# Kernel tuning notes

Hardware: AMD Instinct MI355X
Metric: run time of the kernel (lower is better)

The kernel has to match this reference:

```python
import jax, jax.numpy as jnp
import numpy as np

D_MODEL = 768
EXPAND = 2
D_INNER = EXPAND * D_MODEL  # 1536
D_STATE = 16
D_CONV = 4
DT_RANK = D_MODEL // 16  # 48
N_LAYER = 3
BATCH, SEQLEN = 2, 1024
EPS = 1e-5


def setup_inputs() -> dict:
    key = jax.random.key(0)
    ks = jax.random.split(key, 8)
    s = 0.02
    hidden_states = jax.random.normal(ks[0], (BATCH, SEQLEN, D_MODEL), jnp.float32)
    norm_w = jnp.ones((N_LAYER, D_MODEL), jnp.float32)
    in_proj_w = s * jax.random.normal(ks[1], (N_LAYER, 2 * D_INNER, D_MODEL), jnp.float32)
    conv_w = s * jax.random.normal(ks[2], (N_LAYER, D_INNER, D_CONV), jnp.float32)
    conv_b = jnp.zeros((N_LAYER, D_INNER), jnp.float32)
    x_proj_w = s * jax.random.normal(ks[3], (N_LAYER, DT_RANK + 2 * D_STATE, D_INNER), jnp.float32)
    dt_proj_w = s * jax.random.normal(ks[4], (N_LAYER, D_INNER, DT_RANK), jnp.float32)
    dt_proj_b = jnp.full((N_LAYER, D_INNER), -4.6, jnp.float32)  # softplus ~ 0.01
    # S4D-real init: A_log = log(1..d_state), tiled over channels
    A_log = jnp.tile(jnp.log(jnp.arange(1, D_STATE + 1, dtype=jnp.float32))[None, None, :], (N_LAYER, D_INNER, 1))
    D_skip = jnp.ones((N_LAYER, D_INNER), jnp.float32)
    out_proj_w = s * jax.random.normal(ks[5], (N_LAYER, D_MODEL, D_INNER), jnp.float32)
    norm_f_w = jnp.ones((D_MODEL,), jnp.float32)
    return dict(hidden_states=hidden_states, norm_w=norm_w, in_proj_w=in_proj_w,
                conv_w=conv_w, conv_b=conv_b, x_proj_w=x_proj_w, dt_proj_w=dt_proj_w,
                dt_proj_b=dt_proj_b, A_log=A_log, D_skip=D_skip, out_proj_w=out_proj_w,
                norm_f_w=norm_f_w)


def _rmsnorm(x, w):
    return x * jax.lax.rsqrt(jnp.mean(x * x, axis=-1, keepdims=True) + EPS) * w


def _causal_conv1d(x, w, b):
    # x: [B, L, D]; w: [D, K] depthwise; left-pad for causality
    xt = jnp.transpose(x, (0, 2, 1))  # [B, D, L]
    y = jax.lax.conv_general_dilated(xt, w[:, None, :], window_strides=(1,),
                                     padding=[(D_CONV - 1, 0)], feature_group_count=D_INNER)
    return jnp.transpose(y, (0, 2, 1)) + b


def _selective_scan(u, delta, A, Bc, Cc, Dp):
    # u, delta: [B, L, D]; A: [D, N]; Bc, Cc: [B, L, N]
    def step(h, inp):
        dt, bt, ct, ut = inp  # [B,D], [B,N], [B,N], [B,D]
        h = jnp.exp(dt[..., None] * A) * h + (dt * ut)[..., None] * bt[:, None, :]
        y = jnp.einsum('bdn,bn->bd', h, ct)
        return h, y
    h0 = jnp.zeros((u.shape[0], u.shape[2], A.shape[1]), u.dtype)
    xs = (jnp.swapaxes(delta, 0, 1), jnp.swapaxes(Bc, 0, 1), jnp.swapaxes(Cc, 0, 1), jnp.swapaxes(u, 0, 1))
    _, ys = jax.lax.scan(step, h0, xs)  # ys: [L, B, D]
    return jnp.swapaxes(ys, 0, 1) + u * Dp


def _mixer(h, in_w, cw, cb, xw, dtw, dtb, A_log, Dp, ow):
    xz = jnp.einsum('bld,ed->ble', h, in_w)  # [B, L, 2*D_INNER]
    x, z = xz[..., :D_INNER], xz[..., D_INNER:]
    x = jax.nn.silu(_causal_conv1d(x, cw, cb))
    x_dbl = jnp.einsum('bld,ed->ble', x, xw)
    dt = x_dbl[..., :DT_RANK]
    Bc = x_dbl[..., DT_RANK:DT_RANK + D_STATE]
    Cc = x_dbl[..., DT_RANK + D_STATE:]
    delta = jax.nn.softplus(jnp.einsum('blr,dr->bld', dt, dtw) + dtb)
    A = -jnp.exp(A_log)
    y = _selective_scan(x, delta, A, Bc, Cc, Dp)
    y = y * jax.nn.silu(z)
    return jnp.einsum('bld,ed->ble', y, ow)


def reference(hidden_states, norm_w, in_proj_w, conv_w, conv_b, x_proj_w, dt_proj_w,
              dt_proj_b, A_log, D_skip, out_proj_w, norm_f_w):
    hidden = hidden_states
    residual = None
    for i in range(N_LAYER):
        residual = hidden if residual is None else hidden + residual  # fused add
        hidden = _rmsnorm(residual, norm_w[i])
        hidden = _mixer(hidden, in_proj_w[i], conv_w[i], conv_b[i], x_proj_w[i],
                        dt_proj_w[i], dt_proj_b[i], A_log[i], D_skip[i], out_proj_w[i])
    # final fused add + RMSNorm (prenorm=False)
    return _rmsnorm(hidden + residual, norm_f_w)
```

## Files before the change

kernel.cpp:

```cpp
#include <hip/hip_runtime.h>
#include <math.h>

#define D_MODEL 768
#define D_INNER 1536
#define D_STATE 16
#define D_CONV 4
#define DT_RANK 48
#define N_LAYER 3
#define BATCH 2
#define SEQLEN 1024
#define NROWS (BATCH * SEQLEN)
#define XDBL_W (DT_RANK + 2 * D_STATE)
#define EPS 1e-5f

#define SDN 16
#define NDG (D_INNER / SDN)
#define NSPLIT 4
#define QSTEPS (SEQLEN / NSPLIT)
#define SCLEN2 8
#define KSPLIT_X 8

typedef short bf16x8 __attribute__((ext_vector_type(8)));
typedef float f32x4 __attribute__((ext_vector_type(4)));

__device__ __forceinline__ ushort f2bf(float x) {
    union { float f; uint u; } v; v.f = x;
    uint r = v.u + 0x7fff + ((v.u >> 16) & 1);
    return (ushort)(r >> 16);
}
__device__ __forceinline__ float bf2f(ushort x) {
    union { uint u; float f; } v; v.u = ((uint)x) << 16;
    return v.f;
}

__device__ __forceinline__ void gload_lds16(const void* g, void* l) {
    __builtin_amdgcn_global_load_lds(
        (const __attribute__((address_space(1))) unsigned int*)g,
        (__attribute__((address_space(3))) unsigned int*)l, 16, 0, 0);
}

__global__ __launch_bounds__(256) void cvt_bf16_kernel(
    const float* __restrict__ s, ushort* __restrict__ d, int n4)
{
    int i = blockIdx.x * 256 + threadIdx.x;
    if (i >= n4) return;
    float4 v = ((const float4*)s)[i];
    ushort4 o;
    o.x = f2bf(v.x); o.y = f2bf(v.y); o.z = f2bf(v.z); o.w = f2bf(v.w);
    ((ushort4*)d)[i] = o;
}

__global__ __launch_bounds__(256) void cvt_xw_pad_kernel(
    const float* __restrict__ src, ushort* __restrict__ dst)
{
    const int per = 128 * 1536 / 4;
    int i = blockIdx.x * 256 + threadIdx.x;
    if (i >= 3 * per) return;
    int li = i / per, rem = i - li * per;
    int r = (rem * 4) / 1536, c = (rem * 4) % 1536;
    ushort4 o = make_ushort4(0, 0, 0, 0);
    if (r < XDBL_W) {
        const float* s = src + ((size_t)li * XDBL_W + r) * 1536 + c;
        o.x = f2bf(s[0]); o.y = f2bf(s[1]); o.z = f2bf(s[2]); o.w = f2bf(s[3]);
    }
    ((ushort4*)dst)[i] = o;
}

__global__ __launch_bounds__(256) void cvt_dtw_pad_kernel(
    const float* __restrict__ src, ushort* __restrict__ dst)
{
    const int per = 1536 * 64 / 4;
    int i = blockIdx.x * 256 + threadIdx.x;
    if (i >= 3 * per) return;
    int li = i / per, rem = i - li * per;
    int r = (rem * 4) / 64, c = (rem * 4) % 64;
    ushort4 o = make_ushort4(0, 0, 0, 0);
    if (c < DT_RANK) {
        const float* s = src + ((size_t)li * 1536 + r) * DT_RANK + c;
        o.x = f2bf(s[0]); o.y = f2bf(s[1]); o.z = f2bf(s[2]); o.w = f2bf(s[3]);
    }
    ((ushort4*)dst)[i] = o;
}

__global__ __launch_bounds__(256) void add_rmsnorm_kernel(
    const float* __restrict__ x, const float* __restrict__ res_in,
    const float* __restrict__ w, float* __restrict__ res_out,
    float* __restrict__ normed_f32, ushort* __restrict__ normed_bf)
{
    int row = blockIdx.x;
    int tid = threadIdx.x;
    const float* xr = x + row * D_MODEL;
    float v[3];
    float ss = 0.f;
#pragma unroll
    for (int i = 0; i < 3; i++) {
        int c = tid + i * 256;
        float t = xr[c];
        if (res_in) t += res_in[row * D_MODEL + c];
        v[i] = t;
        ss += t * t;
    }
    for (int off = 32; off; off >>= 1) ss += __shfl_xor(ss, off, 64);
    __shared__ float red[4];
    if ((tid & 63) == 0) red[tid >> 6] = ss;
    __syncthreads();
    float tot = red[0] + red[1] + red[2] + red[3];
    float scale = rsqrtf(tot * (1.f / D_MODEL) + EPS);
#pragma unroll
    for (int i = 0; i < 3; i++) {
        int c = tid + i * 256;
        if (res_out) res_out[row * D_MODEL + c] = v[i];
        float o = v[i] * scale * w[c];
        if (normed_f32) normed_f32[row * D_MODEL + c] = o;
        if (normed_bf)  normed_bf[row * D_MODEL + c] = f2bf(o);
    }
}

template <int BM, int BN, int EPI, int SPLITK, int OUTBF>
__global__ __launch_bounds__(256) void gemm_mfma_kernel(
    const ushort* __restrict__ A, const ushort* __restrict__ W,
    const float* __restrict__ bias, void* __restrict__ Cv,
    int ldc, int Nout, int M, int K)
{
    constexpr int TM = BM / 32;
    constexpr int TN = BN / 32;
    __shared__ __attribute__((aligned(16))) ushort As[BM * 64];
    __shared__ __attribute__((aligned(16))) ushort Ws[BN * 64];
    const int t = threadIdx.x;
    const int lane = t & 63, w = t >> 6;
    const int ln15 = lane & 15, q = lane >> 4;
    const int row0 = blockIdx.y * BM, col0 = blockIdx.x * BN;
    const int wm0 = (w & 1) * (BM / 2), wn0 = (w >> 1) * (BN / 2);

    int kper = K / SPLITK;
    int kz = (SPLITK > 1) ? blockIdx.z * kper : 0;
    float* Cf = (float*)Cv;
    ushort* Cb = (ushort*)Cv;
    if (SPLITK > 1) {
        Cf += (size_t)blockIdx.z * M * ldc;
        Cb += (size_t)blockIdx.z * M * ldc;
    }

    f32x4 acc[TM][TN];
#pragma unroll
    for (int i = 0; i < TM; i++)
#pragma unroll
        for (int j = 0; j < TN; j++) acc[i][j] = (f32x4){0.f, 0.f, 0.f, 0.f};

    for (int k0 = kz; k0 < kz + kper; k0 += 64) {
        __syncthreads();
#pragma unroll
        for (int i = 0; i < BM / 32; i++) {
            int p = (i * 4 + w) * 64 + lane;
            int r = p >> 3, s = p & 7;
            int g = s ^ (r & 7);
            gload_lds16(A + (size_t)(row0 + r) * K + k0 + g * 8, &As[p * 8]);
        }
#pragma unroll
        for (int i = 0; i < BN / 32; i++) {
            int p = (i * 4 + w) * 64 + lane;
            int r = p >> 3, s = p & 7;
            int g = s ^ (r & 7);
            gload_lds16(W + (size_t)(col0 + r) * K + k0 + g * 8, &Ws[p * 8]);
        }
        __syncthreads();
#pragma unroll
        for (int ks = 0; ks < 2; ks++) {
            bf16x8 af[TM], wf[TN];
#pragma unroll
            for (int im = 0; im < TM; im++) {
                int m = wm0 + im * 16 + ln15;
                int slot = (ks * 4 + q) ^ (m & 7);
                af[im] = *(const bf16x8*)&As[m * 64 + slot * 8];
            }
#pragma unroll
            for (int jn = 0; jn < TN; jn++) {
                int n = wn0 + jn * 16 + ln15;
                int slot = (ks * 4 + q) ^ (n & 7);
                wf[jn] = *(const bf16x8*)&Ws[n * 64 + slot * 8];
            }
#pragma unroll
            for (int im = 0; im < TM; im++)
#pragma unroll
                for (int jn = 0; jn < TN; jn++)
                    acc[im][jn] = __builtin_amdgcn_mfma_f32_16x16x32_bf16(
                        af[im], wf[jn], acc[im][jn], 0, 0, 0);
        }
    }
#pragma unroll
    for (int im = 0; im < TM; im++) {
#pragma unroll
        for (int jn = 0; jn < TN; jn++) {
            int rr = row0 + wm0 + im * 16 + q * 4;
            int cc = col0 + wn0 + jn * 16 + ln15;
            if (cc < Nout) {
#pragma unroll
                for (int r = 0; r < 4; r++) {
                    float v = acc[im][jn][r];
                    if (EPI == 1) {
                        v += bias[cc];
                        v = (v > 20.f) ? v : log1pf(__expf(v));
                    }
                    if (OUTBF) Cb[(size_t)(rr + r) * ldc + cc] = f2bf(v);
                    else       Cf[(size_t)(rr + r) * ldc + cc] = v;
                }
            }
        }
    }
}

__global__ __launch_bounds__(256) void xreduce_kernel(
    const float* __restrict__ Cp, float* __restrict__ xdbl,
    ushort* __restrict__ xdt)
{
    const int S4 = NROWS * XDBL_W / 4;
    int i = blockIdx.x * 256 + threadIdx.x;
    if (i >= S4) return;
    const float4* p = (const float4*)Cp;
    float4 o = p[i];
#pragma unroll
    for (int z = 1; z < KSPLIT_X; z++) {
        float4 a = p[i + (size_t)z * S4];
        o.x += a.x; o.y += a.y; o.z += a.z; o.w += a.w;
    }
    ((float4*)xdbl)[i] = o;
    int row = (i * 4) / XDBL_W, c0 = (i * 4) % XDBL_W;
    if (c0 < DT_RANK) {
        ushort4 b;
        b.x = f2bf(o.x); b.y = f2bf(o.y); b.z = f2bf(o.z); b.w = f2bf(o.w);
        *(ushort4*)&xdt[(size_t)row * 64 + c0] = b;
    } else if (c0 < 64) {
        *(ushort4*)&xdt[(size_t)row * 64 + c0] = make_ushort4(0, 0, 0, 0);
    }
}

__global__ __launch_bounds__(256) void conv_silu_kernel(
    const ushort* __restrict__ xzbf, const float* __restrict__ cw,
    const float* __restrict__ cb, float* __restrict__ out,
    ushort* __restrict__ out_bf)
{
    int idx = blockIdx.x * 256 + threadIdx.x;
    int d = idx % D_INNER;
    int bl = idx / D_INNER;
    int l = bl % SEQLEN;
    float s = cb[d];
    const ushort* xp = xzbf + (size_t)bl * (2 * D_INNER) + d;
#pragma unroll
    for (int k = 0; k < D_CONV; k++) {
        int ls = l - (D_CONV - 1) + k;
        if (ls >= 0) s += cw[d * D_CONV + k] * bf2f(xp[(k - (D_CONV - 1)) * (2 * D_INNER)]);
    }
    float sil = s / (1.f + __expf(-s));
    out[(size_t)bl * D_INNER + d] = sil;
    out_bf[(size_t)bl * D_INNER + d] = f2bf(sil);
}

__global__ __launch_bounds__(512) void scanA_kernel(
    const float* __restrict__ u, const float* __restrict__ delta,
    const float* __restrict__ A_log, const float* __restrict__ xdbl,
    float* __restrict__ summ)
{
    __shared__ float PL[8][SDN * 17];
    __shared__ float HL[8][SDN * 17];
    const int t = threadIdx.x;
    const int lane = t & 63;
    const int w = t >> 6;
    const int dsub = lane & 15;
    const int csub = lane >> 4;
    const int bid = blockIdx.x;
    const int qq = bid & 3;
    const int rest = bid >> 2;
    const int b = rest / NDG;
    const int dg = rest % NDG;
    const int d = dg * SDN + dsub;
    const int c = w * 4 + csub;
    const int l0 = qq * QSTEPS + c * SCLEN2;

    float a2[D_STATE];
#pragma unroll
    for (int n = 0; n < D_STATE; n++)
        a2[n] = -__expf(A_log[d * D_STATE + n]) * 1.44269504f;

    const size_t base = (size_t)b * SEQLEN * D_INNER + d;
    const float* dtp = delta + base;
    const float* up  = u + base;
    const float* xrow = xdbl + (size_t)b * SEQLEN * XDBL_W;

    float h[D_STATE], P[D_STATE];
#pragma unroll
    for (int n = 0; n < D_STATE; n++) { h[n] = 0.f; P[n] = 1.f; }

    for (int i = 0; i < SCLEN2; i++) {
        const int l = l0 + i;
        float dt = dtp[(size_t)l * D_INNER];
        float uu = up[(size_t)l * D_INNER];
        const float4* Bv = (const float4*)(xrow + (size_t)l * XDBL_W + DT_RANK);
        float4 q0 = Bv[0], q1 = Bv[1], q2 = Bv[2], q3 = Bv[3];
        float Bf[D_STATE] = {q0.x,q0.y,q0.z,q0.w, q1.x,q1.y,q1.z,q1.w,
                             q2.x,q2.y,q2.z,q2.w, q3.x,q3.y,q3.z,q3.w};
        float dtu = dt * uu;
#pragma unroll
        for (int n = 0; n < D_STATE; n++) {
            float e = __builtin_amdgcn_exp2f(dt * a2[n]);
            P[n] *= e;
            h[n] = e * h[n] + dtu * Bf[n];
        }
    }
#pragma unroll
    for (int n = 0; n < D_STATE; n++) {
        float Pp = __shfl(P[n], lane - 16, 64);
        float Hp = __shfl(h[n], lane - 16, 64);
        bool act = csub >= 1;
        h[n] = act ? P[n] * Hp + h[n] : h[n];
        P[n] = act ? P[n] * Pp : P[n];
    }
#pragma unroll
    for (int n = 0; n < D_STATE; n++) {
        float Pp = __shfl(P[n], lane - 32, 64);
        float Hp = __shfl(h[n], lane - 32, 64);
        bool act = csub >= 2;
        h[n] = act ? P[n] * Hp + h[n] : h[n];
        P[n] = act ? P[n] * Pp : P[n];
    }
    if (csub == 3) {
#pragma unroll
        for (int n = 0; n < D_STATE; n++) {
            PL[w][dsub * 17 + n] = P[n];
            HL[w][dsub * 17 + n] = h[n];
        }
    }
    __syncthreads();
    if (t < SDN * D_STATE) {
        const int d2 = t >> 4, n2 = t & 15;
        float hin = 0.f, pin = 1.f;
        for (int ww = 0; ww < 8; ww++) {
            float Pw = PL[ww][d2 * 17 + n2];
            float Hw = HL[ww][d2 * 17 + n2];
            hin = Pw * hin + Hw;
            pin *= Pw;
        }
        float* so = summ + ((size_t)rest * NSPLIT + qq) * 512;
        so[t] = pin;
        so[256 + t] = hin;
    }
}

__global__ __launch_bounds__(512) void scanC_kernel(
    const float* __restrict__ u, const float* __restrict__ delta,
    const float* __restrict__ A_log, const float* __restrict__ xdbl,
    const float* __restrict__ Dskip, const ushort* __restrict__ xzbf,
    const float* __restrict__ summ, ushort* __restrict__ ybf)
{
    __shared__ float PL[8][SDN * 17];
    __shared__ float HL[8][SDN * 17];
    __shared__ float HIN[256];
    const int t = threadIdx.x;
    const int lane = t & 63;
    const int w = t >> 6;
    const int dsub = lane & 15;
    const int csub = lane >> 4;
    const int bid = blockIdx.x;
    const int qq = bid & 3;
    const int rest = bid >> 2;
    const int b = rest / NDG;
    const int dg = rest % NDG;
    const int d = dg * SDN + dsub;
    const int c = w * 4 + csub;
    const int l0 = qq * QSTEPS + c * SCLEN2;

    if (t < 256) {
        float hin = 0.f;
        for (int z = 0; z < qq; z++) {
            const float* so = summ + ((size_t)rest * NSPLIT + z) * 512;
            hin = so[t] * hin + so[256 + t];
        }
        HIN[t] = hin;
    }

    float a2[D_STATE];
#pragma unroll
    for (int n = 0; n < D_STATE; n++)
        a2[n] = -__expf(A_log[d * D_STATE + n]) * 1.44269504f;

    const size_t base = (size_t)b * SEQLEN * D_INNER + d;
    const float* dtp = delta + base;
    const float* up  = u + base;
    const float* xrow = xdbl + (size_t)b * SEQLEN * XDBL_W;

    float h[D_STATE], P[D_STATE];
#pragma unroll
    for (int n = 0; n < D_STATE; n++) { h[n] = 0.f; P[n] = 1.f; }

    for (int i = 0; i < SCLEN2; i++) {
        const int l = l0 + i;
        float dt = dtp[(size_t)l * D_INNER];
        float uu = up[(size_t)l * D_INNER];
        const float4* Bv = (const float4*)(xrow + (size_t)l * XDBL_W + DT_RANK);
        float4 q0 = Bv[0], q1 = Bv[1], q2 = Bv[2], q3 = Bv[3];
        float Bf[D_STATE] = {q0.x,q0.y,q0.z,q0.w, q1.x,q1.y,q1.z,q1.w,
                             q2.x,q2.y,q2.z,q2.w, q3.x,q3.y,q3.z,q3.w};
        float dtu = dt * uu;
#pragma unroll
        for (int n = 0; n < D_STATE; n++) {
            float e = __builtin_amdgcn_exp2f(dt * a2[n]);
            P[n] *= e;
            h[n] = e * h[n] + dtu * Bf[n];
        }
    }
#pragma unroll
    for (int n = 0; n < D_STATE; n++) {
        float Pp = __shfl(P[n], lane - 16, 64);
        float Hp = __shfl(h[n], lane - 16, 64);
        bool act = csub >= 1;
        h[n] = act ? P[n] * Hp + h[n] : h[n];
        P[n] = act ? P[n] * Pp : P[n];
    }
#pragma unroll
    for (int n = 0; n < D_STATE; n++) {
        float Pp = __shfl(P[n], lane - 32, 64);
        float Hp = __shfl(h[n], lane - 32, 64);
        bool act = csub >= 2;
        h[n] = act ? P[n] * Hp + h[n] : h[n];
        P[n] = act ? P[n] * Pp : P[n];
    }
    if (csub == 3) {
#pragma unroll
        for (int n = 0; n < D_STATE; n++) {
            PL[w][dsub * 17 + n] = P[n];
            HL[w][dsub * 17 + n] = h[n];
        }
    }
    __syncthreads();
    if (t < SDN * D_STATE) {
        const int d2 = t >> 4, n2 = t & 15;
        float hin = HIN[t];
        for (int ww = 0; ww < 8; ww++) {
            float Pw = PL[ww][d2 * 17 + n2];
            float Hw = HL[ww][d2 * 17 + n2];
            HL[ww][d2 * 17 + n2] = hin;
            hin = Pw * hin + Hw;
        }
    }
    __syncthreads();
#pragma unroll
    for (int n = 0; n < D_STATE; n++) {
        float Win = HL[w][dsub * 17 + n];
        float Pe = __shfl(P[n], lane - 16, 64);
        float He = __shfl(h[n], lane - 16, 64);
        h[n] = (csub == 0) ? Win : Pe * Win + He;
    }
    const float Dsk = Dskip[d];
    const ushort* zp = xzbf + (size_t)b * SEQLEN * (2 * D_INNER) + D_INNER + d;
    ushort* yp = ybf + base;
    for (int i = 0; i < SCLEN2; i++) {
        const int l = l0 + i;
        float dt = dtp[(size_t)l * D_INNER];
        float uu = up[(size_t)l * D_INNER];
        float zz = bf2f(zp[(size_t)l * (2 * D_INNER)]);
        const float4* Bv = (const float4*)(xrow + (size_t)l * XDBL_W + DT_RANK);
        float4 q0 = Bv[0], q1 = Bv[1], q2 = Bv[2], q3 = Bv[3];
        float4 r0 = Bv[4], r1 = Bv[5], r2 = Bv[6], r3 = Bv[7];
        float Bf[D_STATE] = {q0.x,q0.y,q0.z,q0.w, q1.x,q1.y,q1.z,q1.w,
                             q2.x,q2.y,q2.z,q2.w, q3.x,q3.y,q3.z,q3.w};
        float Cf[D_STATE] = {r0.x,r0.y,r0.z,r0.w, r1.x,r1.y,r1.z,r1.w,
                             r2.x,r2.y,r2.z,r2.w, r3.x,r3.y,r3.z,r3.w};
        float dtu = dt * uu;
        float acc = 0.f;
#pragma unroll
        for (int n = 0; n < D_STATE; n++) {
            float e = __builtin_amdgcn_exp2f(dt * a2[n]);
            h[n] = e * h[n] + dtu * Bf[n];
            acc += h[n] * Cf[n];
        }
        float yy = acc + uu * Dsk;
        float ee = __builtin_amdgcn_exp2f(-zz * 1.44269504f);
        float sil = zz * __builtin_amdgcn_rcpf(1.f + ee);
        yp[(size_t)l * D_INNER] = f2bf(yy * sil);
    }
}

extern "C" void kernel_launch(void* const* d_in, const int* in_sizes, int n_in,
                              void* d_out, int out_size, void* d_ws, size_t ws_size,
                              hipStream_t stream)
{
    const float* hs        = (const float*)d_in[0];
    const float* norm_w    = (const float*)d_in[1];
    const float* in_proj_w = (const float*)d_in[2];
    const float* conv_w    = (const float*)d_in[3];
    const float* conv_b    = (const float*)d_in[4];
    const float* x_proj_w  = (const float*)d_in[5];
    const float* dt_proj_w = (const float*)d_in[6];
    const float* dt_proj_b = (const float*)d_in[7];
    const float* A_log     = (const float*)d_in[8];
    const float* D_skip    = (const float*)d_in[9];
    const float* out_proj_w= (const float*)d_in[10];
    const float* norm_f_w  = (const float*)d_in[11];

    float* ws = (float*)d_ws;
    float* residual = ws;
    float* hidden   = residual + NROWS * D_MODEL;
    float* xconv    = hidden + NROWS * D_MODEL;
    float* xdbl     = xconv + NROWS * D_INNER;
    float* delta    = xdbl + NROWS * XDBL_W;
    float* xpart    = delta + NROWS * D_INNER;
    float* summ     = xpart + (size_t)KSPLIT_X * NROWS * XDBL_W;
    ushort* xzbf    = (ushort*)(summ + (size_t)BATCH * NDG * NSPLIT * 512);
    ushort* normbf  = xzbf + (size_t)NROWS * 2 * D_INNER;
    ushort* ybf     = normbf + NROWS * D_MODEL;
    ushort* xconvbf = ybf + NROWS * D_INNER;
    ushort* xdtbf   = xconvbf + NROWS * D_INNER;
    ushort* win_bf  = xdtbf + NROWS * 64;
    ushort* wout_bf = win_bf + (size_t)N_LAYER * 2 * D_INNER * D_MODEL;
    ushort* xw_pad  = wout_bf + (size_t)N_LAYER * D_MODEL * D_INNER;
    ushort* dtw_pad = xw_pad + (size_t)N_LAYER * 128 * 1536;

    {
        int n_in4  = N_LAYER * 2 * D_INNER * D_MODEL / 4;
        int n_out4 = N_LAYER * D_MODEL * D_INNER / 4;
        cvt_bf16_kernel<<<(n_in4 + 255) / 256, 256, 0, stream>>>(in_proj_w, win_bf, n_in4);
        cvt_bf16_kernel<<<(n_out4 + 255) / 256, 256, 0, stream>>>(out_proj_w, wout_bf, n_out4);
        cvt_xw_pad_kernel<<<(3 * 128 * 1536 / 4 + 255) / 256, 256, 0, stream>>>(x_proj_w, xw_pad);
        cvt_dtw_pad_kernel<<<(3 * 1536 * 64 / 4 + 255) / 256, 256, 0, stream>>>(dt_proj_w, dtw_pad);
    }

    for (int i = 0; i < N_LAYER; i++) {
        add_rmsnorm_kernel<<<NROWS, 256, 0, stream>>>(
            i == 0 ? hs : hidden, i == 0 ? nullptr : residual,
            norm_w + i * D_MODEL, residual, nullptr, normbf);
        gemm_mfma_kernel<64, 128, 0, 1, 1><<<dim3(2 * D_INNER / 128, NROWS / 64), 256, 0, stream>>>(
            normbf, win_bf + (size_t)i * 2 * D_INNER * D_MODEL, nullptr,
            xzbf, 2 * D_INNER, 2 * D_INNER, NROWS, D_MODEL);
        conv_silu_kernel<<<NROWS * D_INNER / 256, 256, 0, stream>>>(
            xzbf, conv_w + i * D_INNER * D_CONV, conv_b + i * D_INNER, xconv, xconvbf);
        gemm_mfma_kernel<64, 128, 0, KSPLIT_X, 0><<<dim3(1, NROWS / 64, KSPLIT_X), 256, 0, stream>>>(
            xconvbf, xw_pad + (size_t)i * 128 * 1536, nullptr,
            xpart, XDBL_W, XDBL_W, NROWS, D_INNER);
        xreduce_kernel<<<(NROWS * XDBL_W / 4 + 255) / 256, 256, 0, stream>>>(
            xpart, xdbl, xdtbf);
        gemm_mfma_kernel<64, 128, 1, 1, 0><<<dim3(D_INNER / 128, NROWS / 64), 256, 0, stream>>>(
            xdtbf, dtw_pad + (size_t)i * 1536 * 64, dt_proj_b + i * D_INNER,
            delta, D_INNER, D_INNER, NROWS, 64);
        scanA_kernel<<<BATCH * NDG * NSPLIT, 512, 0, stream>>>(
            xconv, delta, A_log + (size_t)i * D_INNER * D_STATE, xdbl, summ);
        scanC_kernel<<<BATCH * NDG * NSPLIT, 512, 0, stream>>>(
            xconv, delta, A_log + (size_t)i * D_INNER * D_STATE, xdbl,
            D_skip + i * D_INNER, xzbf, summ, ybf);
        gemm_mfma_kernel<64, 64, 0, 1, 0><<<dim3(D_MODEL / 64, NROWS / 64), 256, 0, stream>>>(
            ybf, wout_bf + (size_t)i * D_MODEL * D_INNER, nullptr,
            hidden, D_MODEL, D_MODEL, NROWS, D_INNER);
    }
    add_rmsnorm_kernel<<<NROWS, 256, 0, stream>>>(
        hidden, residual, norm_f_w, nullptr, (float*)d_out, nullptr);
}
```

Before: 510.5 us.

## Fuse two-pass selective scan into one cooperative kernel with grid sync

Merges the chunk-summary scan pass and the final scan pass into a single cooperative kernel that keeps per-thread state in registers across a grid-wide sync, so the first chunk recurrence is not recomputed. The scan input u is now read from the bf16 conv output, and the fp32 conv output buffer and its store are removed. This cuts one launch, redundant exp work and memory traffic, but needs all 768 blocks of 512 threads co-resident, and it reads u at bf16 precision.

```diff
diff --git a/kernel.cpp b/kernel.cpp
--- a/kernel.cpp
+++ b/kernel.cpp
@@ -1,5 +1,8 @@
 #include <hip/hip_runtime.h>
+#include <hip/hip_cooperative_groups.h>
 #include <math.h>
+
+namespace cg = cooperative_groups;
 
 #define D_MODEL 768
 #define D_INNER 1536
@@ -236,8 +239,7 @@
 
 __global__ __launch_bounds__(256) void conv_silu_kernel(
     const ushort* __restrict__ xzbf, const float* __restrict__ cw,
-    const float* __restrict__ cb, float* __restrict__ out,
-    ushort* __restrict__ out_bf)
+    const float* __restrict__ cb, ushort* __restrict__ out_bf)
 {
     int idx = blockIdx.x * 256 + threadIdx.x;
     int d = idx % D_INNER;
@@ -251,14 +253,14 @@
         if (ls >= 0) s += cw[d * D_CONV + k] * bf2f(xp[(k - (D_CONV - 1)) * (2 * D_INNER)]);
     }
     float sil = s / (1.f + __expf(-s));
-    out[(size_t)bl * D_INNER + d] = sil;
     out_bf[(size_t)bl * D_INNER + d] = f2bf(sil);
 }
 
-__global__ __launch_bounds__(512) void scanA_kernel(
-    const float* __restrict__ u, const float* __restrict__ delta,
+__global__ __launch_bounds__(512, 6) void scan_coop_kernel(
+    const ushort* __restrict__ ubf, const float* __restrict__ delta,
     const float* __restrict__ A_log, const float* __restrict__ xdbl,
-    float* __restrict__ summ)
+    const float* __restrict__ Dskip, const ushort* __restrict__ xzbf,
+    float* __restrict__ summ, ushort* __restrict__ ybf)
 {
     __shared__ float PL[8][SDN * 17];
     __shared__ float HL[8][SDN * 17];
@@ -283,7 +285,7 @@
 
     const size_t base = (size_t)b * SEQLEN * D_INNER + d;
     const float* dtp = delta + base;
-    const float* up  = u + base;
+    const ushort* up = ubf + base;
     const float* xrow = xdbl + (size_t)b * SEQLEN * XDBL_W;
 
     float h[D_STATE], P[D_STATE];
@@ -293,7 +295,7 @@
     for (int i = 0; i < SCLEN2; i++) {
         const int l = l0 + i;
         float dt = dtp[(size_t)l * D_INNER];
-        float uu = up[(size_t)l * D_INNER];
+        float uu = bf2f(up[(size_t)l * D_INNER]);
         const float4* Bv = (const float4*)(xrow + (size_t)l * XDBL_W + DT_RANK);
         float4 q0 = Bv[0], q1 = Bv[1], q2 = Bv[2], q3 = Bv[3];
         float Bf[D_STATE] = {q0.x,q0.y,q0.z,q0.w, q1.x,q1.y,q1.z,q1.w,
@@ -330,6 +332,7 @@
         }
     }
     __syncthreads();
+
     if (t < SDN * D_STATE) {
         const int d2 = t >> 4, n2 = t & 15;
         float hin = 0.f, pin = 1.f;
@@ -343,97 +346,16 @@
         so[t] = pin;
         so[256 + t] = hin;
     }
-}
-
-__global__ __launch_bounds__(512) void scanC_kernel(
-    const float* __restrict__ u, const float* __restrict__ delta,
-    const float* __restrict__ A_log, const float* __restrict__ xdbl,
-    const float* __restrict__ Dskip, const ushort* __restrict__ xzbf,
-    const float* __restrict__ summ, ushort* __restrict__ ybf)
-{
-    __shared__ float PL[8][SDN * 17];
-    __shared__ float HL[8][SDN * 17];
-    __shared__ float HIN[256];
-    const int t = threadIdx.x;
-    const int lane = t & 63;
-    const int w = t >> 6;
-    const int dsub = lane & 15;
-    const int csub = lane >> 4;
-    const int bid = blockIdx.x;
-    const int qq = bid & 3;
-    const int rest = bid >> 2;
-    const int b = rest / NDG;
-    const int dg = rest % NDG;
-    const int d = dg * SDN + dsub;
-    const int c = w * 4 + csub;
-    const int l0 = qq * QSTEPS + c * SCLEN2;
-
-    if (t < 256) {
+
+    cg::this_grid().sync();
+
+    if (t < SDN * D_STATE) {
+        const int d2 = t >> 4, n2 = t & 15;
         float hin = 0.f;
         for (int z = 0; z < qq; z++) {
             const float* so = summ + ((size_t)rest * NSPLIT + z) * 512;
             hin = so[t] * hin + so[256 + t];
         }
-        HIN[t] = hin;
-    }
-
-    float a2[D_STATE];
-#pragma unroll
-    for (int n = 0; n < D_STATE; n++)
-        a2[n] = -__expf(A_log[d * D_STATE + n]) * 1.44269504f;
-
-    const size_t base = (size_t)b * SEQLEN * D_INNER + d;
-    const float* dtp = delta + base;
-    const float* up  = u + base;
-    const float* xrow = xdbl + (size_t)b * SEQLEN * XDBL_W;
-
-    float h[D_STATE], P[D_STATE];
-#pragma unroll
-    for (int n = 0; n < D_STATE; n++) { h[n] = 0.f; P[n] = 1.f; }
-
-    for (int i = 0; i < SCLEN2; i++) {
-        const int l = l0 + i;
-        float dt = dtp[(size_t)l * D_INNER];
-        float uu = up[(size_t)l * D_INNER];
-        const float4* Bv = (const float4*)(xrow + (size_t)l * XDBL_W + DT_RANK);
-        float4 q0 = Bv[0], q1 = Bv[1], q2 = Bv[2], q3 = Bv[3];
-        float Bf[D_STATE] = {q0.x,q0.y,q0.z,q0.w, q1.x,q1.y,q1.z,q1.w,
-                             q2.x,q2.y,q2.z,q2.w, q3.x,q3.y,q3.z,q3.w};
-        float dtu = dt * uu;
-#pragma unroll
-        for (int n = 0; n < D_STATE; n++) {
-            float e = __builtin_amdgcn_exp2f(dt * a2[n]);
-            P[n] *= e;
-            h[n] = e * h[n] + dtu * Bf[n];
-        }
-    }
-#pragma unroll
-    for (int n = 0; n < D_STATE; n++) {
-        float Pp = __shfl(P[n], lane - 16, 64);
-        float Hp = __shfl(h[n], lane - 16, 64);
-        bool act = csub >= 1;
-        h[n] = act ? P[n] * Hp + h[n] : h[n];
-        P[n] = act ? P[n] * Pp : P[n];
-    }
-#pragma unroll
-    for (int n = 0; n < D_STATE; n++) {
-        float Pp = __shfl(P[n], lane - 32, 64);
-        float Hp = __shfl(h[n], lane - 32, 64);
-        bool act = csub >= 2;
-        h[n] = act ? P[n] * Hp + h[n] : h[n];
-        P[n] = act ? P[n] * Pp : P[n];
-    }
-    if (csub == 3) {
-#pragma unroll
-        for (int n = 0; n < D_STATE; n++) {
-            PL[w][dsub * 17 + n] = P[n];
-            HL[w][dsub * 17 + n] = h[n];
-        }
-    }
-    __syncthreads();
-    if (t < SDN * D_STATE) {
-        const int d2 = t >> 4, n2 = t & 15;
-        float hin = HIN[t];
         for (int ww = 0; ww < 8; ww++) {
             float Pw = PL[ww][d2 * 17 + n2];
             float Hw = HL[ww][d2 * 17 + n2];
@@ -442,6 +364,7 @@
         }
     }
     __syncthreads();
+
 #pragma unroll
     for (int n = 0; n < D_STATE; n++) {
         float Win = HL[w][dsub * 17 + n];
@@ -449,13 +372,14 @@
         float He = __shfl(h[n], lane - 16, 64);
         h[n] = (csub == 0) ? Win : Pe * Win + He;
     }
+
     const float Dsk = Dskip[d];
     const ushort* zp = xzbf + (size_t)b * SEQLEN * (2 * D_INNER) + D_INNER + d;
     ushort* yp = ybf + base;
     for (int i = 0; i < SCLEN2; i++) {
         const int l = l0 + i;
         float dt = dtp[(size_t)l * D_INNER];
-        float uu = up[(size_t)l * D_INNER];
+        float uu = bf2f(up[(size_t)l * D_INNER]);
         float zz = bf2f(zp[(size_t)l * (2 * D_INNER)]);
         const float4* Bv = (const float4*)(xrow + (size_t)l * XDBL_W + DT_RANK);
         float4 q0 = Bv[0], q1 = Bv[1], q2 = Bv[2], q3 = Bv[3];
@@ -499,8 +423,7 @@
     float* ws = (float*)d_ws;
     float* residual = ws;
     float* hidden   = residual + NROWS * D_MODEL;
-    float* xconv    = hidden + NROWS * D_MODEL;
-    float* xdbl     = xconv + NROWS * D_INNER;
+    float* xdbl     = hidden + NROWS * D_MODEL;
     float* delta    = xdbl + NROWS * XDBL_W;
     float* xpart    = delta + NROWS * D_INNER;
     float* summ     = xpart + (size_t)KSPLIT_X * NROWS * XDBL_W;
@@ -531,7 +454,7 @@
             normbf, win_bf + (size_t)i * 2 * D_INNER * D_MODEL, nullptr,
             xzbf, 2 * D_INNER, 2 * D_INNER, NROWS, D_MODEL);
         conv_silu_kernel<<<NROWS * D_INNER / 256, 256, 0, stream>>>(
-            xzbf, conv_w + i * D_INNER * D_CONV, conv_b + i * D_INNER, xconv, xconvbf);
+            xzbf, conv_w + i * D_INNER * D_CONV, conv_b + i * D_INNER, xconvbf);
         gemm_mfma_kernel<64, 128, 0, KSPLIT_X, 0><<<dim3(1, NROWS / 64, KSPLIT_X), 256, 0, stream>>>(
             xconvbf, xw_pad + (size_t)i * 128 * 1536, nullptr,
             xpart, XDBL_W, XDBL_W, NROWS, D_INNER);
@@ -540,11 +463,21 @@
         gemm_mfma_kernel<64, 128, 1, 1, 0><<<dim3(D_INNER / 128, NROWS / 64), 256, 0, stream>>>(
             xdtbf, dtw_pad + (size_t)i * 1536 * 64, dt_proj_b + i * D_INNER,
             delta, D_INNER, D_INNER, NROWS, 64);
-        scanA_kernel<<<BATCH * NDG * NSPLIT, 512, 0, stream>>>(
-            xconv, delta, A_log + (size_t)i * D_INNER * D_STATE, xdbl, summ);
-        scanC_kernel<<<BATCH * NDG * NSPLIT, 512, 0, stream>>>(
-            xconv, delta, A_log + (size_t)i * D_INNER * D_STATE, xdbl,
-            D_skip + i * D_INNER, xzbf, summ, ybf);
+        {
+            const ushort* u_    = xconvbf;
+            const float*  dlt_  = delta;
+            const float*  alog_ = A_log + (size_t)i * D_INNER * D_STATE;
+            const float*  xd_   = xdbl;
+            const float*  dsk_  = D_skip + i * D_INNER;
+            const ushort* xz_   = xzbf;
+            float*        sm_   = summ;
+            ushort*       yb_   = ybf;
+            void* args[] = {(void*)&u_, (void*)&dlt_, (void*)&alog_, (void*)&xd_,
+                            (void*)&dsk_, (void*)&xz_, (void*)&sm_, (void*)&yb_};
+            hipLaunchCooperativeKernel((const void*)scan_coop_kernel,
+                                       dim3(BATCH * NDG * NSPLIT), dim3(512),
+                                       args, 0, stream);
+        }
         gemm_mfma_kernel<64, 64, 0, 1, 0><<<dim3(D_MODEL / 64, NROWS / 64), 256, 0, stream>>>(
             ybf, wout_bf + (size_t)i * D_MODEL * D_INNER, nullptr,
             hidden, D_MODEL, D_MODEL, NROWS, D_INNER);
```

After: 812.1 us. +59.1%, slower.
